# Kernel optimization log

Measured on AMD Instinct MI355X. Metric: run time of the kernel, lower is better.

The kernel has to match this reference:

```python
import jax, jax.numpy as jnp
import numpy as np

B, L, E, H = 2, 2048, 1024, 16
D = E // H

def setup_inputs() -> dict:
    key = jax.random.key(0)
    ks = jax.random.split(key, 6)
    values = jax.random.normal(ks[0], (B, L, E), dtype=jnp.float32)
    keys = jax.random.normal(ks[1], (B, L, E), dtype=jnp.float32)
    query = jax.random.normal(ks[2], (B, L, E), dtype=jnp.float32)
    mask = jax.random.randint(ks[3], (B, 1, L, L), 0, 2, dtype=jnp.int32)
    W_out = jax.random.normal(ks[4], (E, E), dtype=jnp.float32) * 0.02
    b_out = jax.random.normal(ks[5], (E,), dtype=jnp.float32) * 0.02
    return {"values": values, "keys": keys, "query": query, "mask": mask,
            "W_out": W_out, "b_out": b_out}

def reference(values, keys, query, mask, W_out, b_out):
    # Note: source module never applies its per-head q/k/v Linear layers;
    # it only reshapes inputs, so we do the same.
    b, l, e = query.shape
    v = values.reshape(b, l, H, D)   # [B, K, H, D]
    k = keys.reshape(b, l, H, D)     # [B, K, H, D]
    q = query.reshape(b, l, H, D)    # [B, Q, H, D]
    # scores[b,h,q,k] = sum_d q[b,q,h,d] * k[b,k,h,d]
    scores = jnp.einsum('bqhd,bkhd->bhqk', q, k)
    scores = jnp.where(mask == 0, jnp.float32(-1e20), scores)
    # source scales by 1/sqrt(embed_size), not head_dim
    attn = jax.nn.softmax(scores / jnp.float32(E ** 0.5), axis=3)
    out = jnp.einsum('bhqk,bkhd->bqhd', attn, v).reshape(b, l, e)
    out = out @ W_out.T + b_out  # torch Linear: x @ W^T + b
    return out
```

## Files before the change

### kernel.cpp

```cpp
#include <hip/hip_runtime.h>
#include <hip/hip_bf16.h>

typedef __bf16 bf16;
typedef __bf16 bf16x8 __attribute__((ext_vector_type(8)));
typedef __bf16 bf16x4 __attribute__((ext_vector_type(4)));
typedef float  f32x4  __attribute__((ext_vector_type(4)));
typedef float  f32x16 __attribute__((ext_vector_type(16)));

#define B_ 2
#define L_ 2048
#define E_ 1024
#define H_ 16
#define D_ 64

__device__ __forceinline__ int swz(int r, int c) {
    return r * 64 + (((c ^ (r & 7)) & 7) << 3);
}

__device__ __forceinline__ float swap_half(float x, int h) {
#if __has_builtin(__builtin_amdgcn_permlane32_swap)
    typedef unsigned int u32x2 __attribute__((ext_vector_type(2)));
    unsigned int xu = __builtin_bit_cast(unsigned int, x);
    u32x2 r = __builtin_amdgcn_permlane32_swap(xu, xu, false, false);
    return __builtin_bit_cast(float, h ? r.x : r.y);
#else
    return __shfl(x, (((int)threadIdx.x) & 63) ^ 32, 64);
#endif
}

__global__ __launch_bounds__(256) void prep_kernel(const float* __restrict__ v,
                                                   const float* __restrict__ keys,
                                                   const int* __restrict__ mask,
                                                   const float* __restrict__ W,
                                                   bf16* __restrict__ vt,
                                                   bf16* __restrict__ kb,
                                                   unsigned int* __restrict__ mtq2,
                                                   bf16* __restrict__ wb) {
    __shared__ __attribute__((aligned(16))) bf16 tile[64 * 72];
    const int bid = blockIdx.x;
    const int t = threadIdx.x;
    if (bid < 1024) {
        int bh = bid >> 5, b = bh >> 4, h = bh & 15;
        int k0 = (bid & 31) * 64;
        int kk = t >> 2, d0 = (t & 3) * 16;
        const float* src = v + (((size_t)(b * L_ + k0 + kk)) * H_ + h) * D_ + d0;
        float4 f[4];
#pragma unroll
        for (int i = 0; i < 4; i++) f[i] = reinterpret_cast<const float4*>(src)[i];
#pragma unroll
        for (int i = 0; i < 16; i++)
            tile[(d0 + i) * 72 + kk] = (bf16)reinterpret_cast<const float*>(f)[i];
        __syncthreads();
        int dd = t >> 2, c = (t & 3) * 16;
        bf16* dst = vt + ((size_t)bh * 64 + dd) * 2048 + k0 + c;
        *reinterpret_cast<uint4*>(dst)     = *reinterpret_cast<const uint4*>(&tile[dd * 72 + c]);
        *reinterpret_cast<uint4*>(dst + 8) = *reinterpret_cast<const uint4*>(&tile[dd * 72 + c + 8]);
    } else if (bid < 2048) {
        int idx = bid - 1024;
        int b = idx >> 9;
        int q = (idx & 511) * 4 + (t >> 6);
        int li = t & 63;
        const int* mrow = mask + ((size_t)b * L_ + q) * L_;
        unsigned int* mq = mtq2 + (size_t)b * 64 * 2048;
        for (int pass = 0; pass < 32; pass++) {
            int m = mrow[pass * 64 + li];
            unsigned long long bal = __ballot(m & 1);
            if (li == 0) mq[(size_t)(pass * 2) * 2048 + q] = (unsigned int)bal;
            if (li == 1) mq[(size_t)(pass * 2 + 1) * 2048 + q] = (unsigned int)(bal >> 32);
        }
    } else if (bid < 2560) {
        int idx = bid - 2048;
#pragma unroll
        for (int j = 0; j < 8; j++) {
            int i = idx * 2048 + j * 256 + t;
            float4 f = reinterpret_cast<const float4*>(keys)[i];
            bf16x4 o;
            o.x = (bf16)f.x; o.y = (bf16)f.y; o.z = (bf16)f.z; o.w = (bf16)f.w;
            reinterpret_cast<bf16x4*>(kb)[i] = o;
        }
    } else {
        int widx = bid - 2560;
#pragma unroll
        for (int j = 0; j < 16; j++) {
            int i = widx * 4096 + j * 256 + t;
            float4 f = reinterpret_cast<const float4*>(W)[i];
            bf16x4 o;
            o.x = (bf16)f.x; o.y = (bf16)f.y; o.z = (bf16)f.z; o.w = (bf16)f.w;
            reinterpret_cast<bf16x4*>(wb)[i] = o;
        }
    }
}

__global__ __launch_bounds__(256, 4) void attn_kernel(const float* __restrict__ q_,
                                                      const bf16* __restrict__ kb,
                                                      const bf16* __restrict__ vt,
                                                      const unsigned int* __restrict__ mtq2,
                                                      bf16* __restrict__ xb) {
    __shared__ __attribute__((aligned(16))) char smem[27136];
    bf16* Ks = (bf16*)smem;
    bf16* Vs = (bf16*)(smem + 8192);
    bf16* Qs = (bf16*)(smem + 16384);
    unsigned int* Ms32 = (unsigned int*)(smem + 24576);
    float* Om = (float*)smem;
    float* Lrow = (float*)(smem + 16384);
    bf16* Xs = (bf16*)(smem + 17408);

    const int bh = blockIdx.y, b = bh >> 4, hd = bh & 15;
    const int q0 = blockIdx.x * 64;
    const int t = threadIdx.x;
    const int w = t >> 6, lane = t & 63, h = lane >> 5, l31 = lane & 31;
    const int wq = w & 1, wk = w >> 1;
    const int r_ = t >> 2, cq = t & 3;

    const float CSCALE = 1.4426950408889634f / 32.0f;

    {
        const float* src = q_ + ((size_t)(b * L_ + q0 + r_)) * E_ + hd * 64 + cq * 16;
        float4 f[4];
#pragma unroll
        for (int i = 0; i < 4; i++) f[i] = reinterpret_cast<const float4*>(src)[i];
        bf16 tmp[16];
#pragma unroll
        for (int i = 0; i < 16; i++)
            tmp[i] = (bf16)(reinterpret_cast<const float*>(f)[i] * CSCALE);
        *reinterpret_cast<uint4*>(&Qs[swz(r_, cq * 2)])     = *reinterpret_cast<const uint4*>(&tmp[0]);
        *reinterpret_cast<uint4*>(&Qs[swz(r_, cq * 2 + 1)]) = *reinterpret_cast<const uint4*>(&tmp[8]);

        const bf16* ksrc = kb + ((size_t)(b * L_ + r_)) * E_ + hd * 64 + cq * 16;
        *reinterpret_cast<uint4*>(&Ks[swz(r_, cq * 2)])     = *reinterpret_cast<const uint4*>(ksrc);
        *reinterpret_cast<uint4*>(&Ks[swz(r_, cq * 2 + 1)]) = *reinterpret_cast<const uint4*>(ksrc + 8);
        const bf16* vsrc = vt + ((size_t)bh * 64 + r_) * 2048 + cq * 16;
        *reinterpret_cast<uint4*>(&Vs[swz(r_, cq * 2)])     = *reinterpret_cast<const uint4*>(vsrc);
        *reinterpret_cast<uint4*>(&Vs[swz(r_, cq * 2 + 1)]) = *reinterpret_cast<const uint4*>(vsrc + 8);
        if (t < 128)
            Ms32[t] = mtq2[(size_t)(b * 64 + (t >> 6)) * 2048 + q0 + (t & 63)];
    }
    __syncthreads();

    bf16x8 bq[4];
#pragma unroll
    for (int dc = 0; dc < 4; dc++)
        bq[dc] = *reinterpret_cast<const bf16x8*>(&Qs[swz(wq * 32 + l31, dc * 2 + h)]);

    f32x16 oc[2] = {{}, {}};
    float lsum = 0.0f;

    for (int kt = 0; kt < L_ / 64; kt++) {
        uint4 kn0, kn1, vn0, vn1;
        unsigned int mn = 0;
        const bool hasn = (kt + 1) < L_ / 64;
        if (hasn) {
            const int kn = (kt + 1) * 64;
            const bf16* ksrc = kb + ((size_t)(b * L_ + kn + r_)) * E_ + hd * 64 + cq * 16;
            kn0 = *reinterpret_cast<const uint4*>(ksrc);
            kn1 = *reinterpret_cast<const uint4*>(ksrc + 8);
            const bf16* vsrc = vt + ((size_t)bh * 64 + r_) * 2048 + kn + cq * 16;
            vn0 = *reinterpret_cast<const uint4*>(vsrc);
            vn1 = *reinterpret_cast<const uint4*>(vsrc + 8);
            if (t < 128)
                mn = mtq2[(size_t)(b * 64 + (kt + 1) * 2 + (t >> 6)) * 2048 + q0 + (t & 63)];
        }

        f32x16 st = {};
#pragma unroll
        for (int dc = 0; dc < 4; dc++) {
            bf16x8 ak = *reinterpret_cast<const bf16x8*>(&Ks[swz(wk * 32 + l31, dc * 2 + h)]);
            st = __builtin_amdgcn_mfma_f32_32x32x16_bf16(ak, bq[dc], st, 0, 0, 0);
        }

        const unsigned int mwh = Ms32[wk * 64 + wq * 32 + l31] >> (h * 4);
        float pv[16];
#pragma unroll
        for (int i = 0; i < 16; i++) {
            const int base = (i & 3) + 8 * (i >> 2);
            float e = __builtin_amdgcn_exp2f(st[i]);
            pv[i] = ((mwh >> base) & 1u) ? e : 0.0f;
            lsum += pv[i];
        }

        bf16x8 bp[2];
#pragma unroll
        for (int kc = 0; kc < 2; kc++) {
            const int gA = kc * 2, gB = gA + 1;
            float lo[4], hi[4];
#pragma unroll
            for (int r = 0; r < 4; r++) {
                float own  = h ? pv[gB * 4 + r] : pv[gA * 4 + r];
                float send = h ? pv[gA * 4 + r] : pv[gB * 4 + r];
                float recv = swap_half(send, h);
                lo[r] = h ? recv : own;
                hi[r] = h ? own : recv;
            }
            bf16x8 bb;
#pragma unroll
            for (int r = 0; r < 4; r++) { bb[r] = (bf16)lo[r]; bb[4 + r] = (bf16)hi[r]; }
            bp[kc] = bb;
        }

#pragma unroll
        for (int da = 0; da < 2; da++)
#pragma unroll
            for (int kc = 0; kc < 2; kc++) {
                bf16x8 av = *reinterpret_cast<const bf16x8*>(&Vs[swz(da * 32 + l31, wk * 4 + kc * 2 + h)]);
                oc[da] = __builtin_amdgcn_mfma_f32_32x32x16_bf16(av, bp[kc], oc[da], 0, 0, 0);
            }

        __syncthreads();
        if (hasn) {
            *reinterpret_cast<uint4*>(&Ks[swz(r_, cq * 2)])     = kn0;
            *reinterpret_cast<uint4*>(&Ks[swz(r_, cq * 2 + 1)]) = kn1;
            *reinterpret_cast<uint4*>(&Vs[swz(r_, cq * 2)])     = vn0;
            *reinterpret_cast<uint4*>(&Vs[swz(r_, cq * 2 + 1)]) = vn1;
            if (t < 128) Ms32[t] = mn;
        }
        __syncthreads();
    }

    float lw = lsum + swap_half(lsum, h);

    if (wk == 1) {
#pragma unroll
        for (int da = 0; da < 2; da++)
#pragma unroll
            for (int i = 0; i < 16; i++) {
                int d = da * 32 + (i & 3) + 8 * (i >> 2) + 4 * h;
                Om[d * 64 + wq * 32 + l31] = oc[da][i];
            }
        if (h == 0) Lrow[wq * 32 + l31] = lw;
    }
    __syncthreads();
    if (wk == 0) {
        float rinv = 1.0f / (lw + Lrow[wq * 32 + l31]);
#pragma unroll
        for (int da = 0; da < 2; da++)
#pragma unroll
            for (int g = 0; g < 4; g++) {
                int d0 = da * 32 + 8 * g + 4 * h;
                bf16x4 pk;
#pragma unroll
                for (int r = 0; r < 4; r++)
                    pk[r] = (bf16)((oc[da][g * 4 + r] + Om[(d0 + r) * 64 + wq * 32 + l31]) * rinv);
                *reinterpret_cast<bf16x4*>(&Xs[(wq * 32 + l31) * 72 + d0]) = pk;
            }
    }
    __syncthreads();
    {
        bf16* dst = xb + ((size_t)(b * L_ + q0 + r_)) * E_ + hd * 64 + cq * 16;
        *reinterpret_cast<uint4*>(dst)     = *reinterpret_cast<const uint4*>(&Xs[r_ * 72 + cq * 16]);
        *reinterpret_cast<uint4*>(dst + 8) = *reinterpret_cast<const uint4*>(&Xs[r_ * 72 + cq * 16 + 8]);
    }
}

__global__ __launch_bounds__(256, 4) void proj_kernel(const bf16* __restrict__ xb,
                                                      const bf16* __restrict__ wb,
                                                      const float* __restrict__ bias,
                                                      float* __restrict__ out) {
    __shared__ __attribute__((aligned(16))) bf16 As[64 * 64];
    __shared__ __attribute__((aligned(16))) bf16 Bs[64 * 64];
    const int n0 = blockIdx.x * 64, m0 = blockIdx.y * 64;
    const int t = threadIdx.x;
    const int w = t >> 6, lane = t & 63, quad = lane >> 4, ln = lane & 15;
    const int wm = w >> 1, wn = w & 1;

    f32x4 c[2][2];
    const f32x4 zero = {0.f, 0.f, 0.f, 0.f};
#pragma unroll
    for (int mi = 0; mi < 2; mi++)
#pragma unroll
        for (int ni = 0; ni < 2; ni++) c[mi][ni] = zero;

    for (int kt = 0; kt < E_ / 64; kt++) {
        const int k0 = kt * 64;
        {
            const bf16* asrc = xb + (size_t)(m0 + (t >> 2)) * E_ + k0 + (t & 3) * 16;
            const bf16* bsrc = wb + (size_t)(n0 + (t >> 2)) * E_ + k0 + (t & 3) * 16;
            int rr = t >> 2, c4 = (t & 3) * 2;
            *reinterpret_cast<uint4*>(&As[swz(rr, c4)])     = *reinterpret_cast<const uint4*>(asrc);
            *reinterpret_cast<uint4*>(&As[swz(rr, c4 + 1)]) = *reinterpret_cast<const uint4*>(asrc + 8);
            *reinterpret_cast<uint4*>(&Bs[swz(rr, c4)])     = *reinterpret_cast<const uint4*>(bsrc);
            *reinterpret_cast<uint4*>(&Bs[swz(rr, c4 + 1)]) = *reinterpret_cast<const uint4*>(bsrc + 8);
        }
        __syncthreads();
#pragma unroll
        for (int kc = 0; kc < 2; kc++) {
            bf16x8 a[2], bb[2];
#pragma unroll
            for (int mi = 0; mi < 2; mi++)
                a[mi] = *reinterpret_cast<const bf16x8*>(&As[swz(wm * 32 + mi * 16 + ln, kc * 4 + quad)]);
#pragma unroll
            for (int ni = 0; ni < 2; ni++)
                bb[ni] = *reinterpret_cast<const bf16x8*>(&Bs[swz(wn * 32 + ni * 16 + ln, kc * 4 + quad)]);
#pragma unroll
            for (int mi = 0; mi < 2; mi++)
#pragma unroll
                for (int ni = 0; ni < 2; ni++)
                    c[mi][ni] = __builtin_amdgcn_mfma_f32_16x16x32_bf16(a[mi], bb[ni], c[mi][ni], 0, 0, 0);
        }
        __syncthreads();
    }
#pragma unroll
    for (int ni = 0; ni < 2; ni++) {
        float bv = bias[n0 + wn * 32 + ni * 16 + ln];
#pragma unroll
        for (int mi = 0; mi < 2; mi++)
#pragma unroll
            for (int r = 0; r < 4; r++) {
                int row = m0 + wm * 32 + mi * 16 + quad * 4 + r;
                int col = n0 + wn * 32 + ni * 16 + ln;
                out[(size_t)row * E_ + col] = c[mi][ni][r] + bv;
            }
    }
}

extern "C" void kernel_launch(void* const* d_in, const int* in_sizes, int n_in,
                              void* d_out, int out_size, void* d_ws, size_t ws_size,
                              hipStream_t stream) {
    (void)in_sizes; (void)n_in; (void)out_size; (void)ws_size;
    const float* values = (const float*)d_in[0];
    const float* keys   = (const float*)d_in[1];
    const float* query  = (const float*)d_in[2];
    const int*   mask   = (const int*)d_in[3];
    const float* W_out  = (const float*)d_in[4];
    const float* b_out  = (const float*)d_in[5];
    float* out = (float*)d_out;

    char* ws = (char*)d_ws;
    bf16* kb = (bf16*)(ws);
    bf16* vt = (bf16*)(ws + 8388608);
    bf16* wb = (bf16*)(ws + 16777216);
    unsigned int* mtq2 = (unsigned int*)(ws + 18874368);
    bf16* xb = (bf16*)(ws + 19922944);

    prep_kernel<<<2624, 256, 0, stream>>>(values, keys, mask, W_out, vt, kb, mtq2, wb);
    attn_kernel<<<dim3(L_ / 64, B_ * H_), 256, 0, stream>>>(query, kb, vt, mtq2, xb);
    proj_kernel<<<dim3(E_ / 64, (B_ * L_) / 64), 256, 0, stream>>>(xb, wb, b_out, out);
}
```

Before: 213.0 us.

## Pre-tile swizzled K/V/X/W blocks and stream them via global_load_lds double-buffering

The prep kernel now writes K, V (with a permuted column order), W and the attention output as contiguous pre-swizzled 64x64 bf16 tiles. Attention and projection can then copy them straight into LDS with global_load_lds DMA, double-buffered, instead of staging through registers. The V permutation removes the cross-half permlane swap for building P, and mask words are loaded directly per lane. The projection moves to 32x32 MFMA with 128-row tiles. This adds LDS use (about 40 KB and 48 KB) and drops the occupancy hint to 3, and correctness depends on the permuted tile layout matching the MFMA operand layout.

```diff
diff --git a/kernel.cpp b/kernel.cpp
--- a/kernel.cpp
+++ b/kernel.cpp
@@ -17,44 +17,42 @@
     return r * 64 + (((c ^ (r & 7)) & 7) << 3);
 }
 
-__device__ __forceinline__ float swap_half(float x, int h) {
-#if __has_builtin(__builtin_amdgcn_permlane32_swap)
-    typedef unsigned int u32x2 __attribute__((ext_vector_type(2)));
-    unsigned int xu = __builtin_bit_cast(unsigned int, x);
-    u32x2 r = __builtin_amdgcn_permlane32_swap(xu, xu, false, false);
-    return __builtin_bit_cast(float, h ? r.x : r.y);
-#else
-    return __shfl(x, (((int)threadIdx.x) & 63) ^ 32, 64);
-#endif
-}
+#define DMA16(gp, lp)                                                              \
+    __builtin_amdgcn_global_load_lds(                                              \
+        (const __attribute__((address_space(1))) unsigned int*)(gp),               \
+        (__attribute__((address_space(3))) unsigned int*)(lp), 16, 0, 0)
 
 __global__ __launch_bounds__(256) void prep_kernel(const float* __restrict__ v,
                                                    const float* __restrict__ keys,
                                                    const int* __restrict__ mask,
                                                    const float* __restrict__ W,
-                                                   bf16* __restrict__ vt,
-                                                   bf16* __restrict__ kb,
+                                                   bf16* __restrict__ vt_,
+                                                   bf16* __restrict__ kt_,
                                                    unsigned int* __restrict__ mtq2,
-                                                   bf16* __restrict__ wb) {
-    __shared__ __attribute__((aligned(16))) bf16 tile[64 * 72];
+                                                   bf16* __restrict__ wbt) {
+    __shared__ __attribute__((aligned(16))) float tile[64 * 65];
     const int bid = blockIdx.x;
     const int t = threadIdx.x;
     if (bid < 1024) {
-        int bh = bid >> 5, b = bh >> 4, h = bh & 15;
-        int k0 = (bid & 31) * 64;
-        int kk = t >> 2, d0 = (t & 3) * 16;
-        const float* src = v + (((size_t)(b * L_ + k0 + kk)) * H_ + h) * D_ + d0;
+        int bh = bid >> 5, b = bh >> 4, h = bh & 15, kt = bid & 31;
+        int kk = t >> 2, dg = t & 3;
+        const float* src = v + (((size_t)(b * L_ + kt * 64 + kk)) * H_ + h) * D_ + dg * 16;
         float4 f[4];
 #pragma unroll
         for (int i = 0; i < 4; i++) f[i] = reinterpret_cast<const float4*>(src)[i];
 #pragma unroll
         for (int i = 0; i < 16; i++)
-            tile[(d0 + i) * 72 + kk] = (bf16)reinterpret_cast<const float*>(f)[i];
+            tile[(dg * 16 + i) * 65 + kk] = reinterpret_cast<const float*>(f)[i];
         __syncthreads();
-        int dd = t >> 2, c = (t & 3) * 16;
-        bf16* dst = vt + ((size_t)bh * 64 + dd) * 2048 + k0 + c;
-        *reinterpret_cast<uint4*>(dst)     = *reinterpret_cast<const uint4*>(&tile[dd * 72 + c]);
-        *reinterpret_cast<uint4*>(dst + 8) = *reinterpret_cast<const uint4*>(&tile[dd * 72 + c + 8]);
+        int dd = t >> 2, cg = t & 3;
+        const int sig[16] = {0, 1, 2, 3, 8, 9, 10, 11, 4, 5, 6, 7, 12, 13, 14, 15};
+        bf16 tmp[16];
+#pragma unroll
+        for (int p = 0; p < 16; p++)
+            tmp[p] = (bf16)tile[dd * 65 + cg * 16 + sig[p]];
+        bf16* dst = vt_ + ((size_t)bh * 32 + kt) * 4096;
+        *reinterpret_cast<uint4*>(dst + swz(dd, cg * 2))     = *reinterpret_cast<const uint4*>(&tmp[0]);
+        *reinterpret_cast<uint4*>(dst + swz(dd, cg * 2 + 1)) = *reinterpret_cast<const uint4*>(&tmp[8]);
     } else if (bid < 2048) {
         int idx = bid - 1024;
         int b = idx >> 9;
@@ -62,60 +60,79 @@
         int li = t & 63;
         const int* mrow = mask + ((size_t)b * L_ + q) * L_;
         unsigned int* mq = mtq2 + (size_t)b * 64 * 2048;
+#pragma unroll 4
         for (int pass = 0; pass < 32; pass++) {
             int m = mrow[pass * 64 + li];
             unsigned long long bal = __ballot(m & 1);
             if (li == 0) mq[(size_t)(pass * 2) * 2048 + q] = (unsigned int)bal;
             if (li == 1) mq[(size_t)(pass * 2 + 1) * 2048 + q] = (unsigned int)(bal >> 32);
         }
-    } else if (bid < 2560) {
+    } else if (bid < 3072) {
         int idx = bid - 2048;
-#pragma unroll
-        for (int j = 0; j < 8; j++) {
-            int i = idx * 2048 + j * 256 + t;
-            float4 f = reinterpret_cast<const float4*>(keys)[i];
-            bf16x4 o;
-            o.x = (bf16)f.x; o.y = (bf16)f.y; o.z = (bf16)f.z; o.w = (bf16)f.w;
-            reinterpret_cast<bf16x4*>(kb)[i] = o;
-        }
+        int b = idx >> 9, h = (idx >> 5) & 15, kt = idx & 31;
+        int r = t >> 2, cg = t & 3;
+        const float* src = keys + ((size_t)(b * L_ + kt * 64 + r)) * E_ + h * 64 + cg * 16;
+        float4 f[4];
+#pragma unroll
+        for (int i = 0; i < 4; i++) f[i] = reinterpret_cast<const float4*>(src)[i];
+        bf16 tmp[16];
+#pragma unroll
+        for (int i = 0; i < 16; i++)
+            tmp[i] = (bf16)reinterpret_cast<const float*>(f)[i];
+        bf16* dst = kt_ + ((size_t)(b * 16 + h) * 32 + kt) * 4096;
+        *reinterpret_cast<uint4*>(dst + swz(r, cg * 2))     = *reinterpret_cast<const uint4*>(&tmp[0]);
+        *reinterpret_cast<uint4*>(dst + swz(r, cg * 2 + 1)) = *reinterpret_cast<const uint4*>(&tmp[8]);
     } else {
-        int widx = bid - 2560;
-#pragma unroll
-        for (int j = 0; j < 16; j++) {
-            int i = widx * 4096 + j * 256 + t;
-            float4 f = reinterpret_cast<const float4*>(W)[i];
-            bf16x4 o;
-            o.x = (bf16)f.x; o.y = (bf16)f.y; o.z = (bf16)f.z; o.w = (bf16)f.w;
-            reinterpret_cast<bf16x4*>(wb)[i] = o;
-        }
+        int idx = bid - 3072;
+        int n6 = idx >> 4, kt = idx & 15;
+        int r = t >> 2, cg = t & 3;
+        const float* src = W + ((size_t)(n6 * 64 + r)) * E_ + kt * 64 + cg * 16;
+        float4 f[4];
+#pragma unroll
+        for (int i = 0; i < 4; i++) f[i] = reinterpret_cast<const float4*>(src)[i];
+        bf16 tmp[16];
+#pragma unroll
+        for (int i = 0; i < 16; i++)
+            tmp[i] = (bf16)reinterpret_cast<const float*>(f)[i];
+        bf16* dst = wbt + ((size_t)(n6 * 16 + kt)) * 4096;
+        *reinterpret_cast<uint4*>(dst + swz(r, cg * 2))     = *reinterpret_cast<const uint4*>(&tmp[0]);
+        *reinterpret_cast<uint4*>(dst + swz(r, cg * 2 + 1)) = *reinterpret_cast<const uint4*>(&tmp[8]);
     }
 }
 
 __global__ __launch_bounds__(256, 4) void attn_kernel(const float* __restrict__ q_,
-                                                      const bf16* __restrict__ kb,
-                                                      const bf16* __restrict__ vt,
+                                                      const bf16* __restrict__ kt_,
+                                                      const bf16* __restrict__ vt_,
                                                       const unsigned int* __restrict__ mtq2,
-                                                      bf16* __restrict__ xb) {
-    __shared__ __attribute__((aligned(16))) char smem[27136];
-    bf16* Ks = (bf16*)smem;
-    bf16* Vs = (bf16*)(smem + 8192);
-    bf16* Qs = (bf16*)(smem + 16384);
-    unsigned int* Ms32 = (unsigned int*)(smem + 24576);
+                                                      bf16* __restrict__ xbt) {
+    __shared__ __attribute__((aligned(16))) char smem[40960];
+    bf16* Qs = (bf16*)(smem + 32768);
     float* Om = (float*)smem;
     float* Lrow = (float*)(smem + 16384);
-    bf16* Xs = (bf16*)(smem + 17408);
+    bf16* Xs = (bf16*)(smem + 16896);
 
     const int bh = blockIdx.y, b = bh >> 4, hd = bh & 15;
     const int q0 = blockIdx.x * 64;
     const int t = threadIdx.x;
     const int w = t >> 6, lane = t & 63, h = lane >> 5, l31 = lane & 31;
     const int wq = w & 1, wk = w >> 1;
-    const int r_ = t >> 2, cq = t & 3;
+    const int r_ = t >> 2, cg = t & 3;
 
     const float CSCALE = 1.4426950408889634f / 32.0f;
 
+    const bf16* kbase = kt_ + (size_t)bh * 32 * 4096;
+    const bf16* vbase = vt_ + (size_t)bh * 32 * 4096;
+
     {
-        const float* src = q_ + ((size_t)(b * L_ + q0 + r_)) * E_ + hd * 64 + cq * 16;
+        const bf16* gk = kbase + w * 1024 + lane * 8;
+        DMA16(gk, smem + w * 2048);
+        DMA16(gk + 512, smem + w * 2048 + 1024);
+        const bf16* gv = vbase + w * 1024 + lane * 8;
+        DMA16(gv, smem + 16384 + w * 2048);
+        DMA16(gv + 512, smem + 16384 + w * 2048 + 1024);
+    }
+    {
+        const float* src = q_ + ((size_t)(b * L_ + q0 + r_)) * E_ + hd * 64 + cg * 16;
         float4 f[4];
 #pragma unroll
         for (int i = 0; i < 4; i++) f[i] = reinterpret_cast<const float4*>(src)[i];
@@ -123,17 +140,8 @@
 #pragma unroll
         for (int i = 0; i < 16; i++)
             tmp[i] = (bf16)(reinterpret_cast<const float*>(f)[i] * CSCALE);
-        *reinterpret_cast<uint4*>(&Qs[swz(r_, cq * 2)])     = *reinterpret_cast<const uint4*>(&tmp[0]);
-        *reinterpret_cast<uint4*>(&Qs[swz(r_, cq * 2 + 1)]) = *reinterpret_cast<const uint4*>(&tmp[8]);
-
-        const bf16* ksrc = kb + ((size_t)(b * L_ + r_)) * E_ + hd * 64 + cq * 16;
-        *reinterpret_cast<uint4*>(&Ks[swz(r_, cq * 2)])     = *reinterpret_cast<const uint4*>(ksrc);
-        *reinterpret_cast<uint4*>(&Ks[swz(r_, cq * 2 + 1)]) = *reinterpret_cast<const uint4*>(ksrc + 8);
-        const bf16* vsrc = vt + ((size_t)bh * 64 + r_) * 2048 + cq * 16;
-        *reinterpret_cast<uint4*>(&Vs[swz(r_, cq * 2)])     = *reinterpret_cast<const uint4*>(vsrc);
-        *reinterpret_cast<uint4*>(&Vs[swz(r_, cq * 2 + 1)]) = *reinterpret_cast<const uint4*>(vsrc + 8);
-        if (t < 128)
-            Ms32[t] = mtq2[(size_t)(b * 64 + (t >> 6)) * 2048 + q0 + (t & 63)];
+        *reinterpret_cast<uint4*>(&Qs[swz(r_, cg * 2)])     = *reinterpret_cast<const uint4*>(&tmp[0]);
+        *reinterpret_cast<uint4*>(&Qs[swz(r_, cg * 2 + 1)]) = *reinterpret_cast<const uint4*>(&tmp[8]);
     }
     __syncthreads();
 
@@ -145,30 +153,33 @@
     f32x16 oc[2] = {{}, {}};
     float lsum = 0.0f;
 
+    const unsigned int* mbase = mtq2 + (size_t)b * 64 * 2048 + q0 + wq * 32 + l31;
+
     for (int kt = 0; kt < L_ / 64; kt++) {
-        uint4 kn0, kn1, vn0, vn1;
-        unsigned int mn = 0;
-        const bool hasn = (kt + 1) < L_ / 64;
-        if (hasn) {
-            const int kn = (kt + 1) * 64;
-            const bf16* ksrc = kb + ((size_t)(b * L_ + kn + r_)) * E_ + hd * 64 + cq * 16;
-            kn0 = *reinterpret_cast<const uint4*>(ksrc);
-            kn1 = *reinterpret_cast<const uint4*>(ksrc + 8);
-            const bf16* vsrc = vt + ((size_t)bh * 64 + r_) * 2048 + kn + cq * 16;
-            vn0 = *reinterpret_cast<const uint4*>(vsrc);
-            vn1 = *reinterpret_cast<const uint4*>(vsrc + 8);
-            if (t < 128)
-                mn = mtq2[(size_t)(b * 64 + (kt + 1) * 2 + (t >> 6)) * 2048 + q0 + (t & 63)];
-        }
+        __syncthreads();
+        bf16* Kc = (bf16*)(smem + (kt & 1) * 8192);
+        bf16* Vc = (bf16*)(smem + 16384 + (kt & 1) * 8192);
+        if (kt + 1 < L_ / 64) {
+            char* Kn = smem + ((kt + 1) & 1) * 8192;
+            char* Vn = smem + 16384 + ((kt + 1) & 1) * 8192;
+            const bf16* gk = kbase + (size_t)(kt + 1) * 4096 + w * 1024 + lane * 8;
+            DMA16(gk, Kn + w * 2048);
+            DMA16(gk + 512, Kn + w * 2048 + 1024);
+            const bf16* gv = vbase + (size_t)(kt + 1) * 4096 + w * 1024 + lane * 8;
+            DMA16(gv, Vn + w * 2048);
+            DMA16(gv + 512, Vn + w * 2048 + 1024);
+        }
+        unsigned int mw = mbase[(size_t)(kt * 2 + wk) * 2048];
 
         f32x16 st = {};
 #pragma unroll
         for (int dc = 0; dc < 4; dc++) {
-            bf16x8 ak = *reinterpret_cast<const bf16x8*>(&Ks[swz(wk * 32 + l31, dc * 2 + h)]);
+            bf16x8 ak = *reinterpret_cast<const bf16x8*>(&Kc[swz(wk * 32 + l31, dc * 2 + h)]);
             st = __builtin_amdgcn_mfma_f32_32x32x16_bf16(ak, bq[dc], st, 0, 0, 0);
         }
 
-        const unsigned int mwh = Ms32[wk * 64 + wq * 32 + l31] >> (h * 4);
+        const unsigned int mwh = mw >> (h * 4);
+        bf16x8 bp[2];
         float pv[16];
 #pragma unroll
         for (int i = 0; i < 16; i++) {
@@ -177,47 +188,23 @@
             pv[i] = ((mwh >> base) & 1u) ? e : 0.0f;
             lsum += pv[i];
         }
-
-        bf16x8 bp[2];
-#pragma unroll
-        for (int kc = 0; kc < 2; kc++) {
-            const int gA = kc * 2, gB = gA + 1;
-            float lo[4], hi[4];
-#pragma unroll
-            for (int r = 0; r < 4; r++) {
-                float own  = h ? pv[gB * 4 + r] : pv[gA * 4 + r];
-                float send = h ? pv[gA * 4 + r] : pv[gB * 4 + r];
-                float recv = swap_half(send, h);
-                lo[r] = h ? recv : own;
-                hi[r] = h ? own : recv;
-            }
-            bf16x8 bb;
-#pragma unroll
-            for (int r = 0; r < 4; r++) { bb[r] = (bf16)lo[r]; bb[4 + r] = (bf16)hi[r]; }
-            bp[kc] = bb;
-        }
+#pragma unroll
+        for (int kc = 0; kc < 2; kc++)
+#pragma unroll
+            for (int j = 0; j < 8; j++)
+                bp[kc][j] = (bf16)pv[kc * 8 + j];
 
 #pragma unroll
         for (int da = 0; da < 2; da++)
 #pragma unroll
             for (int kc = 0; kc < 2; kc++) {
-                bf16x8 av = *reinterpret_cast<const bf16x8*>(&Vs[swz(da * 32 + l31, wk * 4 + kc * 2 + h)]);
+                bf16x8 av = *reinterpret_cast<const bf16x8*>(&Vc[swz(da * 32 + l31, wk * 4 + kc * 2 + h)]);
                 oc[da] = __builtin_amdgcn_mfma_f32_32x32x16_bf16(av, bp[kc], oc[da], 0, 0, 0);
             }
-
-        __syncthreads();
-        if (hasn) {
-            *reinterpret_cast<uint4*>(&Ks[swz(r_, cq * 2)])     = kn0;
-            *reinterpret_cast<uint4*>(&Ks[swz(r_, cq * 2 + 1)]) = kn1;
-            *reinterpret_cast<uint4*>(&Vs[swz(r_, cq * 2)])     = vn0;
-            *reinterpret_cast<uint4*>(&Vs[swz(r_, cq * 2 + 1)]) = vn1;
-            if (t < 128) Ms32[t] = mn;
-        }
-        __syncthreads();
-    }
-
-    float lw = lsum + swap_half(lsum, h);
-
+    }
+    __syncthreads();
+
+    float lw = lsum + __shfl(lsum, lane ^ 32, 64);
     if (wk == 1) {
 #pragma unroll
         for (int da = 0; da < 2; da++)
@@ -245,71 +232,82 @@
     }
     __syncthreads();
     {
-        bf16* dst = xb + ((size_t)(b * L_ + q0 + r_)) * E_ + hd * 64 + cq * 16;
-        *reinterpret_cast<uint4*>(dst)     = *reinterpret_cast<const uint4*>(&Xs[r_ * 72 + cq * 16]);
-        *reinterpret_cast<uint4*>(dst + 8) = *reinterpret_cast<const uint4*>(&Xs[r_ * 72 + cq * 16 + 8]);
-    }
-}
-
-__global__ __launch_bounds__(256, 4) void proj_kernel(const bf16* __restrict__ xb,
-                                                      const bf16* __restrict__ wb,
+        bf16* xtile = xbt + ((size_t)((b * 32 + (q0 >> 6)) * 16 + hd)) * 4096;
+        *reinterpret_cast<uint4*>(xtile + swz(r_, cg * 2))     = *reinterpret_cast<const uint4*>(&Xs[r_ * 72 + cg * 16]);
+        *reinterpret_cast<uint4*>(xtile + swz(r_, cg * 2 + 1)) = *reinterpret_cast<const uint4*>(&Xs[r_ * 72 + cg * 16 + 8]);
+    }
+}
+
+__global__ __launch_bounds__(256, 3) void proj_kernel(const bf16* __restrict__ xbt,
+                                                      const bf16* __restrict__ wbt,
                                                       const float* __restrict__ bias,
                                                       float* __restrict__ out) {
-    __shared__ __attribute__((aligned(16))) bf16 As[64 * 64];
-    __shared__ __attribute__((aligned(16))) bf16 Bs[64 * 64];
-    const int n0 = blockIdx.x * 64, m0 = blockIdx.y * 64;
+    __shared__ __attribute__((aligned(16))) char smem[49152];
+    const int n0 = blockIdx.x * 64, m0 = blockIdx.y * 128;
     const int t = threadIdx.x;
-    const int w = t >> 6, lane = t & 63, quad = lane >> 4, ln = lane & 15;
+    const int w = t >> 6, lane = t & 63, h = lane >> 5, l31 = lane & 31;
     const int wm = w >> 1, wn = w & 1;
 
-    f32x4 c[2][2];
-    const f32x4 zero = {0.f, 0.f, 0.f, 0.f};
+    const bf16* a0 = xbt + ((size_t)(m0 >> 6)) * 16 * 4096;
+    const bf16* a1 = a0 + 16 * 4096;
+    const bf16* bb_ = wbt + ((size_t)(n0 >> 6)) * 16 * 4096;
+
+    {
+#pragma unroll
+        for (int i = 0; i < 4; i++) {
+            int c = w * 4 + i;
+            const bf16* g = ((c >> 3) ? a1 : a0) + (c & 7) * 512 + lane * 8;
+            DMA16(g, smem + c * 1024);
+        }
+#pragma unroll
+        for (int i = 0; i < 2; i++) {
+            int c = w * 2 + i;
+            DMA16(bb_ + c * 512 + lane * 8, smem + 32768 + c * 1024);
+        }
+    }
+
+    f32x16 acc[2] = {{}, {}};
+    for (int kt = 0; kt < E_ / 64; kt++) {
+        __syncthreads();
+        bf16* Ac = (bf16*)(smem + (kt & 1) * 16384);
+        bf16* Bc = (bf16*)(smem + 32768 + (kt & 1) * 8192);
+        if (kt + 1 < E_ / 64) {
+            char* An = smem + ((kt + 1) & 1) * 16384;
+            char* Bn = smem + 32768 + ((kt + 1) & 1) * 8192;
+            const bf16* an0 = a0 + (kt + 1) * 4096;
+            const bf16* an1 = a1 + (kt + 1) * 4096;
+            const bf16* bn = bb_ + (kt + 1) * 4096;
+#pragma unroll
+            for (int i = 0; i < 4; i++) {
+                int c = w * 4 + i;
+                const bf16* g = ((c >> 3) ? an1 : an0) + (c & 7) * 512 + lane * 8;
+                DMA16(g, An + c * 1024);
+            }
+#pragma unroll
+            for (int i = 0; i < 2; i++) {
+                int c = w * 2 + i;
+                DMA16(bn + c * 512 + lane * 8, Bn + c * 1024);
+            }
+        }
+#pragma unroll
+        for (int dc = 0; dc < 4; dc++) {
+            bf16x8 bfr = *reinterpret_cast<const bf16x8*>(&Bc[swz(wn * 32 + l31, dc * 2 + h)]);
+#pragma unroll
+            for (int mi = 0; mi < 2; mi++) {
+                bf16x8 afr = *reinterpret_cast<const bf16x8*>(&Ac[wm * 4096 + swz(mi * 32 + l31, dc * 2 + h)]);
+                acc[mi] = __builtin_amdgcn_mfma_f32_32x32x16_bf16(afr, bfr, acc[mi], 0, 0, 0);
+            }
+        }
+    }
+
+    float bv = bias[n0 + wn * 32 + l31];
 #pragma unroll
     for (int mi = 0; mi < 2; mi++)
 #pragma unroll
-        for (int ni = 0; ni < 2; ni++) c[mi][ni] = zero;
-
-    for (int kt = 0; kt < E_ / 64; kt++) {
-        const int k0 = kt * 64;
-        {
-            const bf16* asrc = xb + (size_t)(m0 + (t >> 2)) * E_ + k0 + (t & 3) * 16;
-            const bf16* bsrc = wb + (size_t)(n0 + (t >> 2)) * E_ + k0 + (t & 3) * 16;
-            int rr = t >> 2, c4 = (t & 3) * 2;
-            *reinterpret_cast<uint4*>(&As[swz(rr, c4)])     = *reinterpret_cast<const uint4*>(asrc);
-            *reinterpret_cast<uint4*>(&As[swz(rr, c4 + 1)]) = *reinterpret_cast<const uint4*>(asrc + 8);
-            *reinterpret_cast<uint4*>(&Bs[swz(rr, c4)])     = *reinterpret_cast<const uint4*>(bsrc);
-            *reinterpret_cast<uint4*>(&Bs[swz(rr, c4 + 1)]) = *reinterpret_cast<const uint4*>(bsrc + 8);
-        }
-        __syncthreads();
-#pragma unroll
-        for (int kc = 0; kc < 2; kc++) {
-            bf16x8 a[2], bb[2];
-#pragma unroll
-            for (int mi = 0; mi < 2; mi++)
-                a[mi] = *reinterpret_cast<const bf16x8*>(&As[swz(wm * 32 + mi * 16 + ln, kc * 4 + quad)]);
-#pragma unroll
-            for (int ni = 0; ni < 2; ni++)
-                bb[ni] = *reinterpret_cast<const bf16x8*>(&Bs[swz(wn * 32 + ni * 16 + ln, kc * 4 + quad)]);
-#pragma unroll
-            for (int mi = 0; mi < 2; mi++)
-#pragma unroll
-                for (int ni = 0; ni < 2; ni++)
-                    c[mi][ni] = __builtin_amdgcn_mfma_f32_16x16x32_bf16(a[mi], bb[ni], c[mi][ni], 0, 0, 0);
-        }
-        __syncthreads();
-    }
-#pragma unroll
-    for (int ni = 0; ni < 2; ni++) {
-        float bv = bias[n0 + wn * 32 + ni * 16 + ln];
-#pragma unroll
-        for (int mi = 0; mi < 2; mi++)
-#pragma unroll
-            for (int r = 0; r < 4; r++) {
-                int row = m0 + wm * 32 + mi * 16 + quad * 4 + r;
-                int col = n0 + wn * 32 + ni * 16 + ln;
-                out[(size_t)row * E_ + col] = c[mi][ni][r] + bv;
-            }
-    }
+        for (int i = 0; i < 16; i++) {
+            int row = m0 + wm * 64 + mi * 32 + (i & 3) + 8 * (i >> 2) + 4 * h;
+            out[(size_t)row * E_ + n0 + wn * 32 + l31] = acc[mi][i] + bv;
+        }
 }
 
 extern "C" void kernel_launch(void* const* d_in, const int* in_sizes, int n_in,
@@ -325,13 +323,13 @@
     float* out = (float*)d_out;
 
     char* ws = (char*)d_ws;
-    bf16* kb = (bf16*)(ws);
-    bf16* vt = (bf16*)(ws + 8388608);
-    bf16* wb = (bf16*)(ws + 16777216);
+    bf16* vt_ = (bf16*)(ws);
+    bf16* kt_ = (bf16*)(ws + 8388608);
+    bf16* wbt = (bf16*)(ws + 16777216);
     unsigned int* mtq2 = (unsigned int*)(ws + 18874368);
-    bf16* xb = (bf16*)(ws + 19922944);
-
-    prep_kernel<<<2624, 256, 0, stream>>>(values, keys, mask, W_out, vt, kb, mtq2, wb);
-    attn_kernel<<<dim3(L_ / 64, B_ * H_), 256, 0, stream>>>(query, kb, vt, mtq2, xb);
-    proj_kernel<<<dim3(E_ / 64, (B_ * L_) / 64), 256, 0, stream>>>(xb, wb, b_out, out);
-}
+    bf16* xbt = (bf16*)(ws + 19922944);
+
+    prep_kernel<<<3328, 256, 0, stream>>>(values, keys, mask, W_out, vt_, kt_, mtq2, wbt);
+    attn_kernel<<<dim3(L_ / 64, B_ * H_), 256, 0, stream>>>(query, kt_, vt_, mtq2, xbt);
+    proj_kernel<<<dim3(E_ / 64, (B_ * L_) / 128), 256, 0, stream>>>(xbt, wbt, b_out, out);
+}
```

After: 199.8 us. -6.2%, faster.
